# Optimization experiments

Measured on AMD Instinct MI355X. Metric: run time of the kernel, lower is better.

Reference implementation:

```python
import jax, jax.numpy as jnp
import numpy as np

N, M, D = 50000, 32, 128   # nodes, neighbors per node, hidden dim
ROUTING_ITER = 3
EPS = 1e-12                 # matches torch F.normalize default eps


def _l2_normalize(v, axis):
    nrm = jnp.linalg.norm(v, axis=axis, keepdims=True)
    return v / jnp.maximum(nrm, EPS)


def setup_inputs() -> dict:
    key = jax.random.key(0)
    k1, k2 = jax.random.split(key)
    x = jax.random.normal(k1, (N, D), dtype=jnp.float32)
    # 1-indexed neighbor ids, as the module does x[x_nb - 1]
    x_nb = jax.random.randint(k2, (N, M), 1, N + 1, dtype=jnp.int64)
    return {"x": x, "x_nb": x_nb}


def reference(x, x_nb):
    n, d = x.shape
    m = x_nb.shape[1]
    xn = _l2_normalize(x, axis=1)          # (n, d)
    z = xn[x_nb - 1]                        # gather neighbors -> (n, m, d)
    u = None
    for it in range(ROUTING_ITER):
        if u is None:
            p = jnp.zeros((n, m), dtype=x.dtype)
        else:
            p = jnp.einsum('nmd,nd->nm', z, u)      # routing logits
        p = jax.nn.softmax(p, axis=1)               # over neighbors
        u = jnp.einsum('nmd,nm->nd', z, p) + xn     # weighted sum + self
        if it < ROUTING_ITER - 1:
            sq = jnp.sum(u * u, axis=1)             # ||u||^2
            u = (sq / (sq + 1.0))[:, None] * _l2_normalize(u, axis=1)
    return u  # (n, d)
```

## Files before the change

kernel.cpp:

```cpp
#include <hip/hip_runtime.h>


#define M_NB 32
#define D_DIM 128
#define EPSN 1e-12f

typedef float f32x2 __attribute__((ext_vector_type(2)));


__global__ __launch_bounds__(256) void prep_kernel(const float* __restrict__ x,
                                                   unsigned int* __restrict__ xnb,
                                                   float* __restrict__ invn, int n) {
    int row  = (int)((blockIdx.x * blockDim.x + threadIdx.x) >> 6);
    int lane = threadIdx.x & 63;
    if (row >= n) return;
    float2 v = *reinterpret_cast<const float2*>(x + (size_t)row * D_DIM + 2 * lane);
    float s = v.x * v.x + v.y * v.y;
    #pragma unroll
    for (int off = 32; off; off >>= 1) s += __shfl_xor(s, off);
    float inv = 1.0f / fmaxf(sqrtf(s), EPSN);
    if (lane == 0) invn[row] = inv;
    float a = v.x * inv, b = v.y * inv;
    unsigned int ba = __builtin_bit_cast(unsigned int, a);
    unsigned int bb = __builtin_bit_cast(unsigned int, b);
    unsigned int ra = (ba + 0x7fffu + ((ba >> 16) & 1u)) >> 16;
    unsigned int rb = (bb + 0x7fffu + ((bb >> 16) & 1u)) & 0xffff0000u;
    xnb[(size_t)row * 64 + lane] = ra | rb;
}

__global__ __launch_bounds__(256, 4) void routing_bf16_kernel(const float* __restrict__ x,
                                                              const int* __restrict__ nb,
                                                              const unsigned int* __restrict__ xnb,
                                                              const float* __restrict__ invn,
                                                              float* __restrict__ out, int n) {
    int node = (int)((blockIdx.x * blockDim.x + threadIdx.x) >> 6);
    int lane = threadIdx.x & 63;
    if (node >= n) return;
    int g = lane >> 4, t = lane & 15;

    int probe = nb[lane];
    bool sig  = (lane & 1) ? (probe == 0) : (probe != 0);
    bool is64 = __all(sig);

    size_t base = (size_t)node * M_NB + (lane & 31);
    int j = (is64 ? nb[2 * base] : nb[base]) - 1;

    uint4 zp[8];
    #pragma unroll
    for (int i = 0; i < 8; ++i) {
        int jm = __shfl(j, i * 4 + g);
        zp[i] = *reinterpret_cast<const uint4*>(xnb + (size_t)jm * 64 + t * 4);
    }

    f32x2 xn2[4];
    {
        float4 a = *reinterpret_cast<const float4*>(x + (size_t)node * D_DIM + t * 8);
        float4 b = *reinterpret_cast<const float4*>(x + (size_t)node * D_DIM + t * 8 + 4);
        float inv = invn[node];
        xn2[0] = (f32x2){a.x * inv, a.y * inv};
        xn2[1] = (f32x2){a.z * inv, a.w * inv};
        xn2[2] = (f32x2){b.x * inv, b.y * inv};
        xn2[3] = (f32x2){b.z * inv, b.w * inv};
    }

    f32x2 z2[8][4];
    #pragma unroll
    for (int i = 0; i < 8; ++i) {
        unsigned int w[4] = { zp[i].x, zp[i].y, zp[i].z, zp[i].w };
        #pragma unroll
        for (int c = 0; c < 4; ++c) {
            float lo = __builtin_bit_cast(float, w[c] << 16);
            float hi = __builtin_bit_cast(float, w[c] & 0xffff0000u);
            asm volatile("" : "+v"(lo), "+v"(hi));
            z2[i][c] = (f32x2){lo, hi};
        }
    }

    f32x2 u2[4];
    #pragma unroll
    for (int c = 0; c < 4; ++c) {
        f32x2 s = (f32x2){0.f, 0.f};
        #pragma unroll
        for (int i = 0; i < 8; ++i) s += z2[i][c];
        s.x += __shfl_xor(s.x, 16);  s.y += __shfl_xor(s.y, 16);
        s.x += __shfl_xor(s.x, 32);  s.y += __shfl_xor(s.y, 32);
        u2[c] = s * (1.0f / M_NB) + xn2[c];
    }
    {
        f32x2 q = u2[0] * u2[0] + u2[1] * u2[1] + u2[2] * u2[2] + u2[3] * u2[3];
        float sq = q.x + q.y;
        #pragma unroll
        for (int off = 1; off <= 8; off <<= 1) sq += __shfl_xor(sq, off);
        float scale = sq / ((sq + 1.0f) * fmaxf(sqrtf(sq), EPSN));
        #pragma unroll
        for (int c = 0; c < 4; ++c) u2[c] *= scale;
    }

    #pragma unroll
    for (int it = 1; it < 3; ++it) {
        float p[8];
        #pragma unroll
        for (int i = 0; i < 8; ++i) {
            f32x2 a = z2[i][0] * u2[0];
            a += z2[i][1] * u2[1];
            a += z2[i][2] * u2[2];
            a += z2[i][3] * u2[3];
            float pd = a.x + a.y;
            #pragma unroll
            for (int off = 1; off <= 8; off <<= 1) pd += __shfl_xor(pd, off);
            p[i] = pd;
        }
        float mx = p[0];
        #pragma unroll
        for (int i = 1; i < 8; ++i) mx = fmaxf(mx, p[i]);
        mx = fmaxf(mx, __shfl_xor(mx, 16));
        mx = fmaxf(mx, __shfl_xor(mx, 32));
        float sum = 0.f;
        #pragma unroll
        for (int i = 0; i < 8; ++i) { p[i] = __expf(p[i] - mx); sum += p[i]; }
        sum += __shfl_xor(sum, 16);
        sum += __shfl_xor(sum, 32);
        float rs = 1.0f / sum;
        #pragma unroll
        for (int c = 0; c < 4; ++c) {
            f32x2 a = (f32x2){0.f, 0.f};
            #pragma unroll
            for (int i = 0; i < 8; ++i) {
                f32x2 pv = (f32x2){p[i], p[i]};
                a += pv * z2[i][c];
            }
            a.x += __shfl_xor(a.x, 16);  a.y += __shfl_xor(a.y, 16);
            a.x += __shfl_xor(a.x, 32);  a.y += __shfl_xor(a.y, 32);
            u2[c] = a * rs + xn2[c];
        }
        if (it < 2) {
            f32x2 q = u2[0] * u2[0] + u2[1] * u2[1] + u2[2] * u2[2] + u2[3] * u2[3];
            float sq = q.x + q.y;
            #pragma unroll
            for (int off = 1; off <= 8; off <<= 1) sq += __shfl_xor(sq, off);
            float scale = sq / ((sq + 1.0f) * fmaxf(sqrtf(sq), EPSN));
            #pragma unroll
            for (int c = 0; c < 4; ++c) u2[c] *= scale;
        }
    }

    if (g == 0) {
        *reinterpret_cast<float4*>(out + (size_t)node * D_DIM + t * 8) =
            make_float4(u2[0].x, u2[0].y, u2[1].x, u2[1].y);
    } else if (g == 1) {
        *reinterpret_cast<float4*>(out + (size_t)node * D_DIM + t * 8 + 4) =
            make_float4(u2[2].x, u2[2].y, u2[3].x, u2[3].y);
    }
}


__global__ __launch_bounds__(256) void invnorm_kernel(const float* __restrict__ x,
                                                      float* __restrict__ invn, int n) {
    int row  = (int)((blockIdx.x * blockDim.x + threadIdx.x) >> 6);
    int lane = threadIdx.x & 63;
    if (row >= n) return;
    float2 v = *reinterpret_cast<const float2*>(x + (size_t)row * D_DIM + 2 * lane);
    float s = v.x * v.x + v.y * v.y;
    #pragma unroll
    for (int off = 32; off; off >>= 1) s += __shfl_xor(s, off);
    if (lane == 0) invn[row] = 1.0f / fmaxf(sqrtf(s), EPSN);
}

__global__ __launch_bounds__(256) void routing_kernel(const float* __restrict__ x,
                                                      const int* __restrict__ nb,
                                                      const float* __restrict__ invn,
                                                      float* __restrict__ out, int n) {
    int node = (int)((blockIdx.x * blockDim.x + threadIdx.x) >> 6);
    int lane = threadIdx.x & 63;
    if (node >= n) return;

    int probe = nb[lane];
    bool sig  = (lane & 1) ? (probe == 0) : (probe != 0);
    bool is64 = __all(sig);

    size_t base = (size_t)node * M_NB + (lane & 31);
    int j = (is64 ? nb[2 * base] : nb[base]) - 1;
    float vinv = invn[j];

    float2 z[M_NB];
    #pragma unroll
    for (int m = 0; m < M_NB; ++m) {
        int   jm = __shfl(j, m);
        float im = __shfl(vinv, m);
        float2 v = *reinterpret_cast<const float2*>(x + (size_t)jm * D_DIM + 2 * lane);
        z[m] = make_float2(v.x * im, v.y * im);
    }

    float2 xs = *reinterpret_cast<const float2*>(x + (size_t)node * D_DIM + 2 * lane);
    float  si = invn[node];
    float2 xn = make_float2(xs.x * si, xs.y * si);

    float2 u = make_float2(0.f, 0.f);
    #pragma unroll
    for (int m = 0; m < M_NB; ++m) { u.x += z[m].x; u.y += z[m].y; }
    u.x = u.x * (1.0f / M_NB) + xn.x;
    u.y = u.y * (1.0f / M_NB) + xn.y;
    {
        float sq = u.x * u.x + u.y * u.y;
        #pragma unroll
        for (int off = 32; off; off >>= 1) sq += __shfl_xor(sq, off);
        float scale = sq / ((sq + 1.0f) * fmaxf(sqrtf(sq), EPSN));
        u.x *= scale; u.y *= scale;
    }
    #pragma unroll
    for (int it = 1; it < 3; ++it) {
        float p[M_NB];
        #pragma unroll
        for (int m = 0; m < M_NB; ++m) {
            float tt = z[m].x * u.x + z[m].y * u.y;
            #pragma unroll
            for (int off = 32; off; off >>= 1) tt += __shfl_xor(tt, off);
            p[m] = tt;
        }
        float mx = p[0];
        #pragma unroll
        for (int m = 1; m < M_NB; ++m) mx = fmaxf(mx, p[m]);
        float sum = 0.f;
        #pragma unroll
        for (int m = 0; m < M_NB; ++m) { p[m] = __expf(p[m] - mx); sum += p[m]; }
        float rs = 1.0f / sum;
        float2 acc = make_float2(0.f, 0.f);
        #pragma unroll
        for (int m = 0; m < M_NB; ++m) { acc.x += p[m] * z[m].x; acc.y += p[m] * z[m].y; }
        u.x = acc.x * rs + xn.x;
        u.y = acc.y * rs + xn.y;
        if (it < 2) {
            float sq = u.x * u.x + u.y * u.y;
            #pragma unroll
            for (int off = 32; off; off >>= 1) sq += __shfl_xor(sq, off);
            float scale = sq / ((sq + 1.0f) * fmaxf(sqrtf(sq), EPSN));
            u.x *= scale; u.y *= scale;
        }
    }
    *reinterpret_cast<float2*>(out + (size_t)node * D_DIM + 2 * lane) = u;
}

extern "C" void kernel_launch(void* const* d_in, const int* in_sizes, int n_in,
                              void* d_out, int out_size, void* d_ws, size_t ws_size,
                              hipStream_t stream) {
    const float* x  = (const float*)d_in[0];
    const int*   nb = (const int*)d_in[1];
    float* out = (float*)d_out;

    int n = in_sizes[0] / D_DIM;
    int blocks = (n + 3) / 4;

    size_t xnb_bytes = (size_t)n * D_DIM * 2;
    size_t need = xnb_bytes + (size_t)n * 4;

    if (ws_size >= need) {
        unsigned int* xnb = (unsigned int*)d_ws;
        float* invn = (float*)((char*)d_ws + xnb_bytes);
        prep_kernel<<<blocks, 256, 0, stream>>>(x, xnb, invn, n);
        routing_bf16_kernel<<<blocks, 256, 0, stream>>>(x, nb, xnb, invn, out, n);
    } else {
        float* invn = (float*)d_ws;
        invnorm_kernel<<<blocks, 256, 0, stream>>>(x, invn, n);
        routing_kernel<<<blocks, 256, 0, stream>>>(x, nb, invn, out, n);
    }
}
```

Before: 160.7 us.

## Use persistent grid-stride kernels with double-buffered neighbor prefetch in routing

The routing kernel becomes a persistent grid-stride loop over a fixed 2048-block grid. Each wave holds two node slots (A/B) and prefetches the gathered bf16 neighbor rows for the next node while computing the current one, to hide gather latency. The prep kernel now has each half-wave handle one row with float4 loads and a one-row-ahead prefetch. Holding two register buffers raises register pressure, and the launch-bounds occupancy hint (256,4) and the asm register barrier are removed.

```diff
diff --git a/kernel.cpp b/kernel.cpp
--- a/kernel.cpp
+++ b/kernel.cpp
@@ -7,75 +7,83 @@
 
 typedef float f32x2 __attribute__((ext_vector_type(2)));
 
-
-__global__ __launch_bounds__(256) void prep_kernel(const float* __restrict__ x,
-                                                   unsigned int* __restrict__ xnb,
-                                                   float* __restrict__ invn, int n) {
-    int row  = (int)((blockIdx.x * blockDim.x + threadIdx.x) >> 6);
-    int lane = threadIdx.x & 63;
-    if (row >= n) return;
-    float2 v = *reinterpret_cast<const float2*>(x + (size_t)row * D_DIM + 2 * lane);
-    float s = v.x * v.x + v.y * v.y;
-    #pragma unroll
-    for (int off = 32; off; off >>= 1) s += __shfl_xor(s, off);
-    float inv = 1.0f / fmaxf(sqrtf(s), EPSN);
-    if (lane == 0) invn[row] = inv;
-    float a = v.x * inv, b = v.y * inv;
+__device__ __forceinline__ unsigned int pack_bf16(float a, float b) {
     unsigned int ba = __builtin_bit_cast(unsigned int, a);
     unsigned int bb = __builtin_bit_cast(unsigned int, b);
     unsigned int ra = (ba + 0x7fffu + ((ba >> 16) & 1u)) >> 16;
     unsigned int rb = (bb + 0x7fffu + ((bb >> 16) & 1u)) & 0xffff0000u;
-    xnb[(size_t)row * 64 + lane] = ra | rb;
-}
-
-__global__ __launch_bounds__(256, 4) void routing_bf16_kernel(const float* __restrict__ x,
-                                                              const int* __restrict__ nb,
-                                                              const unsigned int* __restrict__ xnb,
-                                                              const float* __restrict__ invn,
-                                                              float* __restrict__ out, int n) {
-    int node = (int)((blockIdx.x * blockDim.x + threadIdx.x) >> 6);
+    return ra | rb;
+}
+
+__global__ __launch_bounds__(256) void prep_kernel(const float* __restrict__ x,
+                                                   unsigned int* __restrict__ xnb,
+                                                   float* __restrict__ invn, int n) {
+    int wid  = (int)((blockIdx.x * blockDim.x + threadIdx.x) >> 6);
     int lane = threadIdx.x & 63;
-    if (node >= n) return;
-    int g = lane >> 4, t = lane & 15;
-
-    int probe = nb[lane];
-    bool sig  = (lane & 1) ? (probe == 0) : (probe != 0);
-    bool is64 = __all(sig);
-
+    int h    = lane >> 5;
+    int l5   = lane & 31;
+    int nw   = (int)((gridDim.x * blockDim.x) >> 6);
+    int stride = nw * 2;
+
+    int row = wid * 2 + h;
+    float4 v = make_float4(0.f, 0.f, 0.f, 0.f);
+    if (row < n) v = *reinterpret_cast<const float4*>(x + (size_t)row * D_DIM + l5 * 4);
+    while (row < n) {
+        int rown = row + stride;
+        float4 vn = make_float4(0.f, 0.f, 0.f, 0.f);
+        if (rown < n) vn = *reinterpret_cast<const float4*>(x + (size_t)rown * D_DIM + l5 * 4);
+        float s = v.x * v.x + v.y * v.y + v.z * v.z + v.w * v.w;
+        #pragma unroll
+        for (int off = 1; off <= 16; off <<= 1) s += __shfl_xor(s, off);
+        float inv = 1.0f / fmaxf(sqrtf(s), EPSN);
+        if (l5 == 0) invn[row] = inv;
+        uint2 w;
+        w.x = pack_bf16(v.x * inv, v.y * inv);
+        w.y = pack_bf16(v.z * inv, v.w * inv);
+        *reinterpret_cast<uint2*>(xnb + (size_t)row * 64 + l5 * 2) = w;
+        row = rown; v = vn;
+    }
+}
+
+
+__device__ __forceinline__ int load_idx(const int* __restrict__ nb, bool is64,
+                                        int node, int lane) {
     size_t base = (size_t)node * M_NB + (lane & 31);
-    int j = (is64 ? nb[2 * base] : nb[base]) - 1;
-
-    uint4 zp[8];
+    return (is64 ? nb[2 * base] : nb[base]) - 1;
+}
+
+__device__ __forceinline__ void load_data(const unsigned int* __restrict__ xnb,
+                                          const float* __restrict__ x,
+                                          const float* __restrict__ invn,
+                                          int node, int j, int g, int t,
+                                          uint4 (&zp)[8], f32x2 (&xn2)[4]) {
     #pragma unroll
     for (int i = 0; i < 8; ++i) {
         int jm = __shfl(j, i * 4 + g);
         zp[i] = *reinterpret_cast<const uint4*>(xnb + (size_t)jm * 64 + t * 4);
     }
-
-    f32x2 xn2[4];
-    {
-        float4 a = *reinterpret_cast<const float4*>(x + (size_t)node * D_DIM + t * 8);
-        float4 b = *reinterpret_cast<const float4*>(x + (size_t)node * D_DIM + t * 8 + 4);
-        float inv = invn[node];
-        xn2[0] = (f32x2){a.x * inv, a.y * inv};
-        xn2[1] = (f32x2){a.z * inv, a.w * inv};
-        xn2[2] = (f32x2){b.x * inv, b.y * inv};
-        xn2[3] = (f32x2){b.z * inv, b.w * inv};
-    }
-
+    float4 a = *reinterpret_cast<const float4*>(x + (size_t)node * D_DIM + t * 8);
+    float4 b = *reinterpret_cast<const float4*>(x + (size_t)node * D_DIM + t * 8 + 4);
+    float inv = invn[node];
+    xn2[0] = (f32x2){a.x * inv, a.y * inv};
+    xn2[1] = (f32x2){a.z * inv, a.w * inv};
+    xn2[2] = (f32x2){b.x * inv, b.y * inv};
+    xn2[3] = (f32x2){b.z * inv, b.w * inv};
+}
+
+__device__ __forceinline__ void compute_store(const uint4 (&zp)[8], const f32x2 (&xn2)[4],
+                                              float* __restrict__ out,
+                                              int node, int g, int t) {
     f32x2 z2[8][4];
     #pragma unroll
     for (int i = 0; i < 8; ++i) {
         unsigned int w[4] = { zp[i].x, zp[i].y, zp[i].z, zp[i].w };
         #pragma unroll
         for (int c = 0; c < 4; ++c) {
-            float lo = __builtin_bit_cast(float, w[c] << 16);
-            float hi = __builtin_bit_cast(float, w[c] & 0xffff0000u);
-            asm volatile("" : "+v"(lo), "+v"(hi));
-            z2[i][c] = (f32x2){lo, hi};
-        }
-    }
-
+            z2[i][c] = (f32x2){ __builtin_bit_cast(float, w[c] << 16),
+                                __builtin_bit_cast(float, w[c] & 0xffff0000u) };
+        }
+    }
     f32x2 u2[4];
     #pragma unroll
     for (int c = 0; c < 4; ++c) {
@@ -95,7 +103,6 @@
         #pragma unroll
         for (int c = 0; c < 4; ++c) u2[c] *= scale;
     }
-
     #pragma unroll
     for (int it = 1; it < 3; ++it) {
         float p[8];
@@ -143,13 +150,54 @@
             for (int c = 0; c < 4; ++c) u2[c] *= scale;
         }
     }
-
     if (g == 0) {
         *reinterpret_cast<float4*>(out + (size_t)node * D_DIM + t * 8) =
             make_float4(u2[0].x, u2[0].y, u2[1].x, u2[1].y);
     } else if (g == 1) {
         *reinterpret_cast<float4*>(out + (size_t)node * D_DIM + t * 8 + 4) =
             make_float4(u2[2].x, u2[2].y, u2[3].x, u2[3].y);
+    }
+}
+
+__global__ __launch_bounds__(256) void routing_bf16_kernel(const float* __restrict__ x,
+                                                           const int* __restrict__ nb,
+                                                           const unsigned int* __restrict__ xnb,
+                                                           const float* __restrict__ invn,
+                                                           float* __restrict__ out, int n) {
+    int wid  = (int)((blockIdx.x * blockDim.x + threadIdx.x) >> 6);
+    int lane = threadIdx.x & 63;
+    int g = lane >> 4, t = lane & 15;
+    int nw  = (int)((gridDim.x * blockDim.x) >> 6);
+    int nw2 = nw * 2;
+
+    int probe = nb[lane];
+    bool sig  = (lane & 1) ? (probe == 0) : (probe != 0);
+    bool is64 = __all(sig);
+
+    int kA = wid;
+    int kB = wid + nw;
+    int jA = 0, jB = 0;
+    uint4 zpA[8], zpB[8];
+    f32x2 xnA[4], xnB[4];
+
+    if (kA < n) {
+        jA = load_idx(nb, is64, kA, lane);
+        load_data(xnb, x, invn, kA, jA, g, t, zpA, xnA);
+    }
+    if (kB < n) jB = load_idx(nb, is64, kB, lane);
+
+    while (kA < n) {
+        if (kB < n) load_data(xnb, x, invn, kB, jB, g, t, zpB, xnB);
+        int kA2 = kA + nw2;
+        if (kA2 < n) jA = load_idx(nb, is64, kA2, lane);
+        compute_store(zpA, xnA, out, kA, g, t);
+        kA = kA2;
+        if (kB >= n) break;
+        if (kA < n) load_data(xnb, x, invn, kA, jA, g, t, zpA, xnA);
+        int kB2 = kB + nw2;
+        if (kB2 < n) jB = load_idx(nb, is64, kB2, lane);
+        compute_store(zpB, xnB, out, kB, g, t);
+        kB = kB2;
     }
 }
 
@@ -248,7 +296,6 @@
     float* out = (float*)d_out;
 
     int n = in_sizes[0] / D_DIM;
-    int blocks = (n + 3) / 4;
 
     size_t xnb_bytes = (size_t)n * D_DIM * 2;
     size_t need = xnb_bytes + (size_t)n * 4;
@@ -256,10 +303,12 @@
     if (ws_size >= need) {
         unsigned int* xnb = (unsigned int*)d_ws;
         float* invn = (float*)((char*)d_ws + xnb_bytes);
+        const int blocks = 2048;
         prep_kernel<<<blocks, 256, 0, stream>>>(x, xnb, invn, n);
         routing_bf16_kernel<<<blocks, 256, 0, stream>>>(x, nb, xnb, invn, out, n);
     } else {
         float* invn = (float*)d_ws;
+        int blocks = (n + 3) / 4;
         invnorm_kernel<<<blocks, 256, 0, stream>>>(x, invn, n);
         routing_kernel<<<blocks, 256, 0, stream>>>(x, nb, invn, out, n);
     }
```

Measured after the change: 189.1 us. 17.7% more time.
